# Optimization experiments

Measured on AMD Instinct MI355X. Metric: run time of the kernel, lower is better.

Reference implementation:

```python
import jax, jax.numpy as jnp
import numpy as np

IGNORE_INDEX = -100


def setup_inputs() -> dict:
    key = jax.random.key(0)
    k1, k2, k3 = jax.random.split(key, 3)
    N, H, V = 4096, 2048, 50257
    x = jax.random.normal(k1, (N, H), dtype=jnp.float32)
    weight = jax.random.normal(k2, (V, H), dtype=jnp.float32) * (1.0 / np.sqrt(H))
    y = jax.random.randint(k3, (N,), 0, V, dtype=jnp.int64)
    return {"x": x, "weight": weight, "y": y}


def reference(x, weight, y):
    # Fused linear + cross entropy: logits = x @ W^T, mean NLL over non-ignored tokens.
    logits = jnp.einsum("nh,vh->nv", x, weight)  # [N, V]
    logp = jax.nn.log_softmax(logits, axis=-1)
    mask = (y != IGNORE_INDEX)
    safe_y = jnp.where(mask, y, 0)
    nll = -jnp.take_along_axis(logp, safe_y[:, None], axis=-1)[:, 0]  # [N]
    n_valid = jnp.maximum(jnp.sum(mask), 1)
    loss = jnp.sum(jnp.where(mask, nll, 0.0)) / n_valid.astype(nll.dtype)
    return loss
```

## Files before the change

kernel.cpp:

```cpp
#include <hip/hip_runtime.h>
#include <hip/hip_bf16.h>
#include <math.h>

typedef unsigned char  u8;
typedef unsigned int   u32;
typedef __attribute__((ext_vector_type(8)))  int   int8v;
typedef __attribute__((ext_vector_type(16))) float f32x16;

#define IGNORE_INDEX (-100)

__device__ __forceinline__ u8 f32_to_e4m3(float f) {
    union { float f; u32 u; } v; v.f = f;
    u32 s  = (v.u >> 24) & 0x80u;
    u32 au = v.u & 0x7FFFFFFFu;
    float a = __uint_as_float(au);
    if (a >= 448.0f) return (u8)(s | 0x7E);
    int e = (int)(au >> 23) - 127;
    if (e >= -6) {
        u32 m    = au & 0x7FFFFFu;
        u32 keep = m >> 20;
        u32 rest = m & 0xFFFFFu;
        keep += (rest > 0x80000u) || (rest == 0x80000u && (keep & 1u));
        u32 code = ((u32)(e + 7) << 3) + keep;
        if (code > 0x7E) code = 0x7E;
        return (u8)(s | code);
    } else {
        int q = (int)rintf(a * 512.0f);
        return (u8)(s | (u32)q);
    }
}

__global__ __launch_bounds__(256) void cvt_pack_fp8(const float* __restrict__ in,
                                                    u8* __restrict__ out,
                                                    float scale, int H, int nRows) {
    __shared__ __align__(16) u8 lds[16384];
    const int kc    = blockIdx.x;
    const int panel = blockIdx.y;
    const int t     = threadIdx.x;

#pragma unroll
    for (int it = 0; it < 4; ++it) {
        int u  = it * 256 + t;
        int r  = u >> 3;
        int cc = u & 7;
        int row = panel * 128 + r;
        u8 tmp[16];
        if (row < nRows) {
            const float* src = in + (size_t)row * H + kc * 128 + cc * 16;
#pragma unroll
            for (int p = 0; p < 4; ++p) {
                float4 f = *(const float4*)(src + p * 4);
                tmp[p * 4 + 0] = f32_to_e4m3(f.x * scale);
                tmp[p * 4 + 1] = f32_to_e4m3(f.y * scale);
                tmp[p * 4 + 2] = f32_to_e4m3(f.z * scale);
                tmp[p * 4 + 3] = f32_to_e4m3(f.w * scale);
            }
        } else {
#pragma unroll
            for (int p = 0; p < 16; ++p) tmp[p] = 0;
        }
        int i2 = r >> 5, ln32 = r & 31;
        int ks = cc >> 2, khalf = (cc >> 1) & 1, h = cc & 1;
        int s  = i2 * 4 + ks * 2 + h;
        int lane = khalf * 32 + ln32;
        *(int4*)(lds + s * 1024 + lane * 16) = *(const int4*)tmp;
    }
    __syncthreads();

    u8* dst = out + ((size_t)panel * gridDim.x + kc) * 16384;
    const int4* l4 = (const int4*)lds;
    int4* d4 = (int4*)dst;
#pragma unroll
    for (int p = 0; p < 4; ++p)
        d4[p * 256 + t] = l4[p * 256 + t];
}

__device__ __forceinline__ void gl_lds16(const u8* g, u8* l) {
    __builtin_amdgcn_global_load_lds(
        (const __attribute__((address_space(1))) void*)g,
        (__attribute__((address_space(3))) void*)l, 16, 0, 0);
}

__global__ __launch_bounds__(512, 2) void gemm_lse_partial(
    const u8* __restrict__ Ap,
    const u8* __restrict__ Bp,
    float2* __restrict__ partials,
    int KC, int V, int VT, int MT)
{
    __shared__ __align__(16) u8 sA3[3][16384];
    __shared__ __align__(16) u8 sB3[3][16384];
    __shared__ float2 red[256 * 4];

    const int tid   = threadIdx.x;
    const int w     = tid >> 6;
    const int lane  = tid & 63;
    const int wm    = w >> 2;
    const int wn    = w & 3;
    const int ln32  = lane & 31;
    const int khalf = lane >> 5;
    const int l16   = lane * 16;

    const int nwg = MT * VT;
    int orig = blockIdx.x;
    int swz  = orig;
    if ((nwg & 7) == 0) { int cpx = nwg >> 3; swz = (orig & 7) * cpx + (orig >> 3); }
    const int bx = swz % MT;
    const int by = swz / MT;
    const int bx2 = bx * 2, by2 = by * 2;

    f32x16 acc[4][2];
#pragma unroll
    for (int i = 0; i < 4; ++i)
#pragma unroll
        for (int j = 0; j < 2; ++j)
#pragma unroll
            for (int r = 0; r < 16; ++r) acc[i][j][r] = 0.0f;

    const int scaleA = 0x7C7C7C7C;
    const int scaleB = 0x7B7B7B7B;

#define MFMA(av, bv, c) __builtin_amdgcn_mfma_scale_f32_32x32x64_f8f6f4(av, bv, c, 0, 0, 0, scaleA, 0, scaleB)

#define STAGE(T_, B_) do { \
    int kc_ = (T_) >> 1, ks_ = (T_) & 1; \
    for (int k_ = 0; k_ < 2; ++k_) { \
        int cA_  = w * 2 + k_; \
        int pnl_ = cA_ >> 3, sub_ = cA_ & 7; \
        int s_   = (sub_ >> 1) * 4 + ks_ * 2 + (sub_ & 1); \
        gl_lds16(Ap + ((size_t)(bx2 + pnl_) * KC + kc_) * 16384 + s_ * 1024 + l16, \
                 &sA3[B_][cA_ * 1024]); \
        gl_lds16(Bp + ((size_t)(by2 + pnl_) * KC + kc_) * 16384 + s_ * 1024 + l16, \
                 &sB3[B_][cA_ * 1024]); \
    } } while (0)

#define LDF(dst, base, off) do { \
    int4 lo_ = *(const int4*)((base) + (off) + l16); \
    int4 hi_ = *(const int4*)((base) + (off) + 1024 + l16); \
    dst[0]=lo_.x; dst[1]=lo_.y; dst[2]=lo_.z; dst[3]=lo_.w; \
    dst[4]=hi_.x; dst[5]=hi_.y; dst[6]=hi_.z; dst[7]=hi_.w; } while (0)

    const int aOff = wm * 8192;
    const int bOff = (wn >> 1) * 8192 + (wn & 1) * 4096;

    const int T = KC * 2;
    STAGE(0, 0);
    STAGE(1, 1);
    asm volatile("s_waitcnt vmcnt(4)\n\ts_barrier" ::: "memory");

    int cur = 0;
#pragma unroll 1
    for (int t = 0; t < T; ++t) {
        const u8* bA = &sA3[cur][0];
        const u8* bB = &sB3[cur][0];
        int8v a0, a1, a2, a3, b0v, b1v;
        LDF(a0, bA, aOff);           LDF(a1, bA, aOff + 2048);
        LDF(a2, bA, aOff + 4096);    LDF(a3, bA, aOff + 6144);
        LDF(b0v, bB, bOff);          LDF(b1v, bB, bOff + 2048);

        int nb = cur + 2; if (nb >= 3) nb -= 3;
        if (t + 2 < T) STAGE(t + 2, nb);

        __builtin_amdgcn_s_setprio(1);
        acc[0][0] = MFMA(a0, b0v, acc[0][0]); acc[0][1] = MFMA(a0, b1v, acc[0][1]);
        acc[1][0] = MFMA(a1, b0v, acc[1][0]); acc[1][1] = MFMA(a1, b1v, acc[1][1]);
        acc[2][0] = MFMA(a2, b0v, acc[2][0]); acc[2][1] = MFMA(a2, b1v, acc[2][1]);
        acc[3][0] = MFMA(a3, b0v, acc[3][0]); acc[3][1] = MFMA(a3, b1v, acc[3][1]);
        __builtin_amdgcn_s_setprio(0);

        if (t + 2 < T) asm volatile("s_waitcnt vmcnt(4) lgkmcnt(0)\n\ts_barrier" ::: "memory");
        else           asm volatile("s_waitcnt vmcnt(0) lgkmcnt(0)\n\ts_barrier" ::: "memory");
        cur = cur + 1; if (cur >= 3) cur -= 3;
    }

    bool vj0 = (by * 256 + wn * 64 + ln32)      < V;
    bool vj1 = (by * 256 + wn * 64 + 32 + ln32) < V;

#pragma unroll
    for (int i2 = 0; i2 < 4; ++i2) {
#pragma unroll
        for (int r = 0; r < 16; ++r) {
            float x0 = vj0 ? acc[i2][0][r] : -INFINITY;
            float x1 = vj1 ? acc[i2][1][r] : -INFINITY;
            float m = fmaxf(x0, x1);
#pragma unroll
            for (int o = 1; o < 32; o <<= 1)
                m = fmaxf(m, __shfl_xor(m, o, 64));
            float s = 0.0f;
            if (vj0) s += __expf(acc[i2][0][r] - m);
            if (vj1) s += __expf(acc[i2][1][r] - m);
#pragma unroll
            for (int o = 1; o < 32; o <<= 1)
                s += __shfl_xor(s, o, 64);
            if (ln32 == 0) {
                int row = wm * 128 + i2 * 32 + (r & 3) + 8 * (r >> 2) + 4 * khalf;
                red[row * 4 + wn] = make_float2(m, s);
            }
        }
    }
    __syncthreads();

    if (tid < 256) {
        float m = -INFINITY, s = 0.0f;
#pragma unroll
        for (int q = 0; q < 4; ++q) {
            float2 p = red[tid * 4 + q];
            float nm = fmaxf(m, p.x);
            s = s * __expf(m - nm) + p.y * __expf(p.x - nm);
            m = nm;
        }
        partials[(size_t)(bx * 256 + tid) * VT + by] = make_float2(m, s);
    }
#undef MFMA
#undef STAGE
#undef LDF
}

__global__ __launch_bounds__(256) void row_final(
    const float* __restrict__ x,
    const float* __restrict__ W,
    const int* __restrict__ y,
    const float2* __restrict__ partials,
    float* __restrict__ nll, float* __restrict__ valid,
    int H, int V, int VT)
{
    const int n = blockIdx.x;
    const int t = threadIdx.x;
    const int yn = y[n];
    const bool ok = (yn != IGNORE_INDEX);

    float dsum = 0.0f;
    if (ok) {
        int cy = yn; if (cy < 0) cy = 0; if (cy >= V) cy = V - 1;
        const float4* xr = (const float4*)(x + (size_t)n * H);
        const float4* wr = (const float4*)(W + (size_t)cy * H);
        int nf4 = H >> 2;
        for (int i = t; i < nf4; i += 256) {
            float4 a = xr[i], b = wr[i];
            dsum += a.x * b.x + a.y * b.y + a.z * b.z + a.w * b.w;
        }
    }

    float m = -INFINITY, s = 0.0f;
    const float2* pr = partials + (size_t)n * VT;
    for (int i = t; i < VT; i += 256) {
        float2 p = pr[i];
        float nm = fmaxf(m, p.x);
        s = s * __expf(m - nm) + p.y * __expf(p.x - nm);
        m = nm;
    }

    __shared__ float rm[256], rs[256], rd[256];
    rm[t] = m; rs[t] = s; rd[t] = dsum;
    __syncthreads();
    for (int o = 128; o > 0; o >>= 1) {
        if (t < o) {
            float m2 = rm[t + o], s2 = rs[t + o];
            float nm = fmaxf(rm[t], m2);
            rs[t] = rs[t] * __expf(rm[t] - nm) + s2 * __expf(m2 - nm);
            rm[t] = nm;
            rd[t] += rd[t + o];
        }
        __syncthreads();
    }
    if (t == 0) {
        float lse = rm[0] + __logf(rs[0]);
        nll[n]   = ok ? (lse - rd[0]) : 0.0f;
        valid[n] = ok ? 1.0f : 0.0f;
    }
}

__global__ __launch_bounds__(1024) void final_loss(
    const float* __restrict__ nll, const float* __restrict__ valid,
    float* __restrict__ out, int n)
{
    __shared__ float ss[1024], sv[1024];
    const int t = threadIdx.x;
    float a = 0.0f, b = 0.0f;
    for (int i = t; i < n; i += 1024) { a += nll[i]; b += valid[i]; }
    ss[t] = a; sv[t] = b;
    __syncthreads();
    for (int o = 512; o > 0; o >>= 1) {
        if (t < o) { ss[t] += ss[t + o]; sv[t] += sv[t + o]; }
        __syncthreads();
    }
    if (t == 0) out[0] = ss[0] / fmaxf(sv[0], 1.0f);
}

extern "C" void kernel_launch(void* const* d_in, const int* in_sizes, int n_in,
                              void* d_out, int out_size, void* d_ws, size_t ws_size,
                              hipStream_t stream) {
    const float* x = (const float*)d_in[0];
    const float* W = (const float*)d_in[1];
    const int*   y = (const int*)d_in[2];

    const long xsz = in_sizes[0];
    const long wsz = in_sizes[1];
    const int  N   = in_sizes[2];
    const int  H   = (int)(xsz / N);
    const int  V   = (int)(wsz / H);
    const int  VT  = (V + 255) / 256;
    const int  PV  = VT * 2;
    const int  MT  = N / 256;
    const int  PM  = N / 128;
    const int  KC  = H / 128;

    char* ws = (char*)d_ws;
    size_t off = 0;
    u8* Wp = (u8*)(ws + off); off += (size_t)PV * KC * 16384; off = (off + 255) & ~(size_t)255;
    u8* Xp = (u8*)(ws + off); off += (size_t)PM * KC * 16384; off = (off + 255) & ~(size_t)255;
    float2* partials = (float2*)(ws + off); off += (size_t)N * VT * sizeof(float2); off = (off + 255) & ~(size_t)255;
    float* nll   = (float*)(ws + off); off += (size_t)N * 4;
    float* valid = (float*)(ws + off); off += (size_t)N * 4;

    cvt_pack_fp8<<<dim3(KC, PV), 256, 0, stream>>>(W, Wp, 16.0f, H, V);
    cvt_pack_fp8<<<dim3(KC, PM), 256, 0, stream>>>(x, Xp, 8.0f, H, N);

    gemm_lse_partial<<<dim3(MT * VT), dim3(512), 0, stream>>>(Xp, Wp, partials, KC, V, VT, MT);

    row_final<<<N, 256, 0, stream>>>(x, W, y, partials, nll, valid, H, V, VT);
    final_loss<<<1, 1024, 0, stream>>>(nll, valid, (float*)d_out, N);
}
```

Before: 1.333 ms.

## Restructure FP8 GEMM into double-buffered four-phase pipeline and use hardware FP8 conversion

The GEMM main loop now works on one full K chunk per iteration, using two 64KB LDS buffers instead of a triple ring. Each iteration is split into four phases, and each phase interleaves LDS fragment reads, async global-to-LDS prefetch of the next chunk, and MFMA groups, separated by barriers. The goal is to hide load latency behind matrix work with a finer-grained, ping-pong style schedule, at the cost of more barriers and a larger LDS footprint. Separately, the fp32-to-e4m3 packing kernel uses the hardware packed FP8 convert builtin when it is available. This replaces the bit-manipulation software rounding, but saturation and rounding behaviour may differ slightly.

```diff
diff --git a/kernel.cpp b/kernel.cpp
--- a/kernel.cpp
+++ b/kernel.cpp
@@ -30,6 +30,19 @@
     }
 }
 
+__device__ __forceinline__ u32 cvt4_e4m3(float4 f, float scale) {
+#if __has_builtin(__builtin_amdgcn_cvt_pk_fp8_f32)
+    int pk = 0;
+    pk = __builtin_amdgcn_cvt_pk_fp8_f32(f.x * scale, f.y * scale, pk, false);
+    pk = __builtin_amdgcn_cvt_pk_fp8_f32(f.z * scale, f.w * scale, pk, true);
+    return (u32)pk;
+#else
+    u32 b0 = f32_to_e4m3(f.x * scale), b1 = f32_to_e4m3(f.y * scale);
+    u32 b2 = f32_to_e4m3(f.z * scale), b3 = f32_to_e4m3(f.w * scale);
+    return b0 | (b1 << 8) | (b2 << 16) | (b3 << 24);
+#endif
+}
+
 __global__ __launch_bounds__(256) void cvt_pack_fp8(const float* __restrict__ in,
                                                     u8* __restrict__ out,
                                                     float scale, int H, int nRows) {
@@ -44,20 +57,15 @@
         int r  = u >> 3;
         int cc = u & 7;
         int row = panel * 128 + r;
-        u8 tmp[16];
+        u32 tmp[4];
         if (row < nRows) {
             const float* src = in + (size_t)row * H + kc * 128 + cc * 16;
 #pragma unroll
-            for (int p = 0; p < 4; ++p) {
-                float4 f = *(const float4*)(src + p * 4);
-                tmp[p * 4 + 0] = f32_to_e4m3(f.x * scale);
-                tmp[p * 4 + 1] = f32_to_e4m3(f.y * scale);
-                tmp[p * 4 + 2] = f32_to_e4m3(f.z * scale);
-                tmp[p * 4 + 3] = f32_to_e4m3(f.w * scale);
-            }
+            for (int p = 0; p < 4; ++p)
+                tmp[p] = cvt4_e4m3(*(const float4*)(src + p * 4), scale);
         } else {
 #pragma unroll
-            for (int p = 0; p < 16; ++p) tmp[p] = 0;
+            for (int p = 0; p < 4; ++p) tmp[p] = 0;
         }
         int i2 = r >> 5, ln32 = r & 31;
         int ks = cc >> 2, khalf = (cc >> 1) & 1, h = cc & 1;
@@ -87,8 +95,7 @@
     float2* __restrict__ partials,
     int KC, int V, int VT, int MT)
 {
-    __shared__ __align__(16) u8 sA3[3][16384];
-    __shared__ __align__(16) u8 sB3[3][16384];
+    __shared__ __align__(16) u8 smem[2][65536];
     __shared__ float2 red[256 * 4];
 
     const int tid   = threadIdx.x;
@@ -121,16 +128,17 @@
 
 #define MFMA(av, bv, c) __builtin_amdgcn_mfma_scale_f32_32x32x64_f8f6f4(av, bv, c, 0, 0, 0, scaleA, 0, scaleB)
 
-#define STAGE(T_, B_) do { \
-    int kc_ = (T_) >> 1, ks_ = (T_) & 1; \
-    for (int k_ = 0; k_ < 2; ++k_) { \
-        int cA_  = w * 2 + k_; \
-        int pnl_ = cA_ >> 3, sub_ = cA_ & 7; \
-        int s_   = (sub_ >> 1) * 4 + ks_ * 2 + (sub_ & 1); \
-        gl_lds16(Ap + ((size_t)(bx2 + pnl_) * KC + kc_) * 16384 + s_ * 1024 + l16, \
-                 &sA3[B_][cA_ * 1024]); \
-        gl_lds16(Bp + ((size_t)(by2 + pnl_) * KC + kc_) * 16384 + s_ * 1024 + l16, \
-                 &sB3[B_][cA_ * 1024]); \
+#define STAGE2(kc_, ks_, d_, l0_) do { \
+    _Pragma("unroll") \
+    for (int l_ = (l0_); l_ < (l0_) + 2; ++l_) { \
+        int c_  = w * 4 + l_; \
+        int isB_ = c_ >> 4, cc_ = c_ & 15; \
+        int pnl_ = cc_ >> 3, sub_ = cc_ & 7; \
+        int s_  = (sub_ >> 1) * 4 + (ks_) * 2 + (sub_ & 1); \
+        const u8* src_ = (isB_ ? (Bp + ((size_t)(by2 + pnl_) * KC + (kc_)) * 16384) \
+                               : (Ap + ((size_t)(bx2 + pnl_) * KC + (kc_)) * 16384)) \
+                         + s_ * 1024 + l16; \
+        gl_lds16(src_, &smem[d_][isB_ * 32768 + (ks_) * 16384 + cc_ * 1024]); \
     } } while (0)
 
 #define LDF(dst, base, off) do { \
@@ -139,37 +147,71 @@
     dst[0]=lo_.x; dst[1]=lo_.y; dst[2]=lo_.z; dst[3]=lo_.w; \
     dst[4]=hi_.x; dst[5]=hi_.y; dst[6]=hi_.z; dst[7]=hi_.w; } while (0)
 
-    const int aOff = wm * 8192;
-    const int bOff = (wn >> 1) * 8192 + (wn & 1) * 4096;
-
-    const int T = KC * 2;
-    STAGE(0, 0);
-    STAGE(1, 1);
-    asm volatile("s_waitcnt vmcnt(4)\n\ts_barrier" ::: "memory");
+#define LDA(dst, i2_, ks_) LDF(dst, &smem[cur][0], (ks_)*16384 + wm*8192 + (i2_)*2048)
+#define LDB(dst, j_, ks_)  LDF(dst, &smem[cur][0], 32768 + (ks_)*16384 + (wn>>1)*8192 + ((wn&1)*2+(j_))*2048)
+
+#define BARRIER asm volatile("s_barrier" ::: "memory")
+#define LGKM0   asm volatile("s_waitcnt lgkmcnt(0)" ::: "memory")
+
+    const int T = KC;
+    STAGE2(0, 0, 0, 0); STAGE2(0, 0, 0, 2);
+    STAGE2(0, 1, 0, 0); STAGE2(0, 1, 0, 2);
+    if (T > 1) {
+        STAGE2(1, 0, 1, 0); STAGE2(1, 0, 1, 2);
+        asm volatile("s_waitcnt vmcnt(8)" ::: "memory");
+    } else {
+        asm volatile("s_waitcnt vmcnt(4)" ::: "memory");
+    }
+    BARRIER;
 
     int cur = 0;
 #pragma unroll 1
     for (int t = 0; t < T; ++t) {
-        const u8* bA = &sA3[cur][0];
-        const u8* bB = &sB3[cur][0];
+        const int nxt = cur ^ 1;
         int8v a0, a1, a2, a3, b0v, b1v;
-        LDF(a0, bA, aOff);           LDF(a1, bA, aOff + 2048);
-        LDF(a2, bA, aOff + 4096);    LDF(a3, bA, aOff + 6144);
-        LDF(b0v, bB, bOff);          LDF(b1v, bB, bOff + 2048);
-
-        int nb = cur + 2; if (nb >= 3) nb -= 3;
-        if (t + 2 < T) STAGE(t + 2, nb);
-
+
+        LDB(b0v, 0, 0); LDB(b1v, 1, 0); LDA(a0, 0, 0); LDA(a1, 1, 0);
+        if (t + 1 < T) STAGE2(t + 1, 1, nxt, 0);
+        BARRIER; LGKM0;
         __builtin_amdgcn_s_setprio(1);
         acc[0][0] = MFMA(a0, b0v, acc[0][0]); acc[0][1] = MFMA(a0, b1v, acc[0][1]);
         acc[1][0] = MFMA(a1, b0v, acc[1][0]); acc[1][1] = MFMA(a1, b1v, acc[1][1]);
+        __builtin_amdgcn_s_setprio(0);
+        BARRIER;
+
+        LDA(a2, 2, 0); LDA(a3, 3, 0);
+        if (t + 1 < T) STAGE2(t + 1, 1, nxt, 2);
+        BARRIER; LGKM0;
+        __builtin_amdgcn_s_setprio(1);
         acc[2][0] = MFMA(a2, b0v, acc[2][0]); acc[2][1] = MFMA(a2, b1v, acc[2][1]);
         acc[3][0] = MFMA(a3, b0v, acc[3][0]); acc[3][1] = MFMA(a3, b1v, acc[3][1]);
         __builtin_amdgcn_s_setprio(0);
-
-        if (t + 2 < T) asm volatile("s_waitcnt vmcnt(4) lgkmcnt(0)\n\ts_barrier" ::: "memory");
-        else           asm volatile("s_waitcnt vmcnt(0) lgkmcnt(0)\n\ts_barrier" ::: "memory");
-        cur = cur + 1; if (cur >= 3) cur -= 3;
+        if (t + 1 < T) asm volatile("s_waitcnt vmcnt(8)" ::: "memory");
+        else           asm volatile("s_waitcnt vmcnt(0)" ::: "memory");
+        BARRIER;
+
+        LDB(b0v, 0, 1); LDB(b1v, 1, 1); LDA(a0, 0, 1); LDA(a1, 1, 1);
+        if (t + 2 < T) STAGE2(t + 2, 0, cur, 0);
+        BARRIER; LGKM0;
+        __builtin_amdgcn_s_setprio(1);
+        acc[0][0] = MFMA(a0, b0v, acc[0][0]); acc[0][1] = MFMA(a0, b1v, acc[0][1]);
+        acc[1][0] = MFMA(a1, b0v, acc[1][0]); acc[1][1] = MFMA(a1, b1v, acc[1][1]);
+        __builtin_amdgcn_s_setprio(0);
+        BARRIER;
+
+        LDA(a2, 2, 1); LDA(a3, 3, 1);
+        if (t + 2 < T) STAGE2(t + 2, 0, cur, 2);
+        BARRIER; LGKM0;
+        __builtin_amdgcn_s_setprio(1);
+        acc[2][0] = MFMA(a2, b0v, acc[2][0]); acc[2][1] = MFMA(a2, b1v, acc[2][1]);
+        acc[3][0] = MFMA(a3, b0v, acc[3][0]); acc[3][1] = MFMA(a3, b1v, acc[3][1]);
+        __builtin_amdgcn_s_setprio(0);
+        if (t + 2 < T)      asm volatile("s_waitcnt vmcnt(8)" ::: "memory");
+        else if (t + 1 < T) asm volatile("s_waitcnt vmcnt(4)" ::: "memory");
+        else                asm volatile("s_waitcnt vmcnt(0)" ::: "memory");
+        BARRIER;
+
+        cur = nxt;
     }
 
     bool vj0 = (by * 256 + wn * 64 + ln32)      < V;
@@ -211,8 +253,12 @@
         partials[(size_t)(bx * 256 + tid) * VT + by] = make_float2(m, s);
     }
 #undef MFMA
-#undef STAGE
+#undef STAGE2
 #undef LDF
+#undef LDA
+#undef LDB
+#undef BARRIER
+#undef LGKM0
 }
 
 __global__ __launch_bounds__(256) void row_final(
```

After: 1.462 ms. +9.7%, slower.
